# Kernel optimization log

Hardware: AMD Instinct MI355X
Metric: run time of the kernel (lower is better)

Reference implementation:

```python
import jax, jax.numpy as jnp
import numpy as np

VERY_NEG = -1e30


def setup_inputs() -> dict:
    key = jax.random.key(0)
    kq, kk, kv, km = jax.random.split(key, 4)
    B, H, S, D = 4, 8, 2048, 64
    Q = jax.random.normal(kq, (B, H, S, D), dtype=jnp.float32)
    K = jax.random.normal(kk, (B, H, S, D), dtype=jnp.float32)
    V = jax.random.normal(kv, (B, H, S, D), dtype=jnp.float32)
    # key-padding mask broadcast over heads and queries: 1 = keep, 0 = masked
    mask = jax.random.randint(km, (B, 1, 1, S), 0, 2, dtype=jnp.int32)
    return {"Q": Q, "K": K, "V": V, "mask": mask}


def reference(Q, K, V, mask):
    d_k = Q.shape[-1]
    scale = jnp.asarray(np.power(d_k, 0.5), dtype=Q.dtype)
    # scores: [B,H,S_q,S_k]
    scores = jnp.einsum("bhqd,bhkd->bhqk", Q, K) / scale
    # QANet exponential_mask: add -1e30 where mask == 0
    masked = scores + (1.0 - mask.astype(scores.dtype)) * VERY_NEG
    attn = jax.nn.softmax(masked, axis=-1)
    out = jnp.einsum("bhqk,bhkd->bhqd", attn, V)
    return out
```

## Files before the change

### kernel.cpp

```cpp
#include <hip/hip_runtime.h>

typedef _Float16 half8_t __attribute__((ext_vector_type(8)));
typedef _Float16 half4_t __attribute__((ext_vector_type(4)));
typedef _Float16 half2_t __attribute__((ext_vector_type(2)));
typedef __fp16 fp16x2 __attribute__((ext_vector_type(2)));
typedef float f32x4 __attribute__((ext_vector_type(4)));

#define S_LEN 2048
#define D_DIM 64
#define SD (S_LEN * D_DIM)
#define BC 64
#define NKT (S_LEN / BC)
#define LDK 72
#define LDO 68
#define THR 4.0f
#define WS_NEED ((size_t)16 * 1024 * 1024)

__global__ __launch_bounds__(256)
void prep_kernel(const float* __restrict__ Kg, const float* __restrict__ Vg,
                 _Float16* __restrict__ wsK, _Float16* __restrict__ wsV) {
  __shared__ float vt[64][68];
  const int blk = blockIdx.x;
  const int t = threadIdx.x;

  if (blk < 1024) {
    const int bh = blk >> 5, kt = blk & 31;
    const float* src = Kg + (size_t)bh * SD + (size_t)kt * BC * D_DIM;
    char* dst = (char*)wsK + (size_t)blk * 8192;
#pragma unroll
    for (int i = 0; i < 2; ++i) {
      int task = t + 256 * i;
      int row = task >> 3, j = task & 7;
      float4 lo = *(const float4*)(src + row * D_DIM + 8 * j);
      float4 hi = *(const float4*)(src + row * D_DIM + 8 * j + 4);
      fp16x2 p0 = __builtin_amdgcn_cvt_pkrtz(lo.x, lo.y);
      fp16x2 p1 = __builtin_amdgcn_cvt_pkrtz(lo.z, lo.w);
      fp16x2 p2 = __builtin_amdgcn_cvt_pkrtz(hi.x, hi.y);
      fp16x2 p3 = __builtin_amdgcn_cvt_pkrtz(hi.z, hi.w);
      half8_t h;
      h[0] = (_Float16)p0[0]; h[1] = (_Float16)p0[1];
      h[2] = (_Float16)p1[0]; h[3] = (_Float16)p1[1];
      h[4] = (_Float16)p2[0]; h[5] = (_Float16)p2[1];
      h[6] = (_Float16)p3[0]; h[7] = (_Float16)p3[1];
      *(half8_t*)(dst + row * 128 + ((16 * j) ^ ((row & 7) << 4))) = h;
    }
  } else {
    const int vb = blk - 1024;
    const int bh = vb >> 5, kt = vb & 31;
    const float* src = Vg + (size_t)bh * SD + (size_t)kt * BC * D_DIM;
#pragma unroll
    for (int i = 0; i < 4; ++i) {
      int r = (t >> 4) + 16 * i, c4 = t & 15;
      *(float4*)&vt[r][c4 * 4] = *(const float4*)(src + r * D_DIM + c4 * 4);
    }
    __syncthreads();
    char* dst = (char*)wsV + (size_t)vb * 8192;
#pragma unroll
    for (int i = 0; i < 4; ++i) {
      int task = t + 256 * i;
      int drow = task >> 4, j2 = task & 15, k0 = 4 * j2;
      float a = vt[k0][drow], b = vt[k0 + 1][drow];
      float cc = vt[k0 + 2][drow], d = vt[k0 + 3][drow];
      fp16x2 h0 = __builtin_amdgcn_cvt_pkrtz(a, b);
      fp16x2 h1 = __builtin_amdgcn_cvt_pkrtz(cc, d);
      half4_t h;
      h[0] = (_Float16)h0[0]; h[1] = (_Float16)h0[1];
      h[2] = (_Float16)h1[0]; h[3] = (_Float16)h1[1];
      *(half4_t*)(dst + drow * 128 + ((8 * j2) ^ ((drow & 15) << 3))) = h;
    }
  }
}

__global__ __launch_bounds__(256, 2)
void fattn_dma(const float* __restrict__ Qg, const _Float16* __restrict__ wsK,
               const _Float16* __restrict__ wsV, const int* __restrict__ Mg,
               float* __restrict__ Og) {
  __shared__ __align__(16) char smem[40960];
  float* Msh = (float*)(smem + 32768);
  float* Osh = (float*)smem;

  const int t = threadIdx.x;
  const int w = t >> 6;
  const int lane = t & 63;
  const int g = lane >> 4;
  const int c = lane & 15;

  const int bh = blockIdx.x & 31;
  const int qt = blockIdx.x >> 5;
  const int qb = qt * 128;

  const float* Qb = Qg + (size_t)bh * SD;
  const int*   Mb = Mg + (size_t)(bh >> 3) * S_LEN;
  float*       Ob = Og + (size_t)bh * SD;

  {
    int4 m0 = *(const int4*)(Mb + 8 * t);
    int4 m1 = *(const int4*)(Mb + 8 * t + 4);
    float4 f0, f1;
    f0.x = (float)(m0.x - 1) * 1e30f; f0.y = (float)(m0.y - 1) * 1e30f;
    f0.z = (float)(m0.z - 1) * 1e30f; f0.w = (float)(m0.w - 1) * 1e30f;
    f1.x = (float)(m1.x - 1) * 1e30f; f1.y = (float)(m1.y - 1) * 1e30f;
    f1.z = (float)(m1.z - 1) * 1e30f; f1.w = (float)(m1.w - 1) * 1e30f;
    *(float4*)(Msh + 8 * t) = f0;
    *(float4*)(Msh + 8 * t + 4) = f1;
  }

  const float qscale = 0.125f * 1.44269504088896340736f;
  half8_t qf[2][2];
#pragma unroll
  for (int h = 0; h < 2; ++h) {
    const float* qp = Qb + (size_t)(qb + 32 * w + 16 * h + c) * D_DIM + 8 * g;
#pragma unroll
    for (int ks = 0; ks < 2; ++ks) {
      float4 lo = *(const float4*)(qp + 32 * ks);
      float4 hi = *(const float4*)(qp + 32 * ks + 4);
      fp16x2 p0 = __builtin_amdgcn_cvt_pkrtz(lo.x * qscale, lo.y * qscale);
      fp16x2 p1 = __builtin_amdgcn_cvt_pkrtz(lo.z * qscale, lo.w * qscale);
      fp16x2 p2 = __builtin_amdgcn_cvt_pkrtz(hi.x * qscale, hi.y * qscale);
      fp16x2 p3 = __builtin_amdgcn_cvt_pkrtz(hi.z * qscale, hi.w * qscale);
      half8_t hh;
      hh[0] = (_Float16)p0[0]; hh[1] = (_Float16)p0[1];
      hh[2] = (_Float16)p1[0]; hh[3] = (_Float16)p1[1];
      hh[4] = (_Float16)p2[0]; hh[5] = (_Float16)p2[1];
      hh[6] = (_Float16)p3[0]; hh[7] = (_Float16)p3[1];
      qf[h][ks] = hh;
    }
  }

  const size_t tile_base0 = (size_t)bh * 32 * 8192;
  auto dma = [&](int buf, int kt) {
    const char* gK = (const char*)wsK + tile_base0 + (size_t)kt * 8192 +
                     w * 2048 + lane * 16;
    const char* gV = (const char*)wsV + tile_base0 + (size_t)kt * 8192 +
                     w * 2048 + lane * 16;
    char* lK = smem + 8192 * buf + w * 2048;
    char* lV = smem + 16384 + 8192 * buf + w * 2048;
    __builtin_amdgcn_global_load_lds((const float*)gK, (float*)lK, 16, 0, 0);
    __builtin_amdgcn_global_load_lds((const float*)(gK + 1024), (float*)(lK + 1024), 16, 0, 0);
    __builtin_amdgcn_global_load_lds((const float*)gV, (float*)lV, 16, 0, 0);
    __builtin_amdgcn_global_load_lds((const float*)(gV + 1024), (float*)(lV + 1024), 16, 0, 0);
  };

  f32x4 acc[2][4];
  f32x4 accl[2];
#pragma unroll
  for (int h = 0; h < 2; ++h) {
#pragma unroll
    for (int j = 0; j < 4; ++j) accl[h][j] = 0.f;
#pragma unroll
    for (int i = 0; i < 4; ++i)
#pragma unroll
      for (int j = 0; j < 4; ++j) acc[h][i][j] = 0.f;
  }
  float mrun[2] = {-1e30f, -1e30f};

  half4_t ones4;
  ones4[0] = (_Float16)1.0f; ones4[1] = (_Float16)1.0f;
  ones4[2] = (_Float16)1.0f; ones4[3] = (_Float16)1.0f;

  const int kxor = (c & 7) << 4;
  const int vxor = c << 3;

  dma(0, 0);
  __syncthreads();

  for (int kt = 0; kt < NKT; ++kt) {
    const int cur = kt & 1;
    if (kt < NKT - 1) dma(cur ^ 1, kt + 1);

    const char* Kc = smem + 8192 * cur;
    const char* Vc = smem + 16384 + 8192 * cur;

    f32x4 sT[2][4];
    __builtin_amdgcn_s_setprio(1);
#pragma unroll
    for (int mt = 0; mt < 4; ++mt) {
      f32x4 z0, z1;
#pragma unroll
      for (int j = 0; j < 4; ++j) { z0[j] = 0.f; z1[j] = 0.f; }
#pragma unroll
      for (int ks = 0; ks < 2; ++ks) {
        half8_t kf = *(const half8_t*)(Kc + (16 * mt + c) * 128 +
                                       ((ks * 64 + g * 16) ^ kxor));
        z0 = __builtin_amdgcn_mfma_f32_16x16x32_f16(kf, qf[0][ks], z0, 0, 0, 0);
        z1 = __builtin_amdgcn_mfma_f32_16x16x32_f16(kf, qf[1][ks], z1, 0, 0, 0);
      }
      sT[0][mt] = z0;
      sT[1][mt] = z1;
    }
    __builtin_amdgcn_s_setprio(0);

    half4_t vf[4][4];
#pragma unroll
    for (int dt = 0; dt < 4; ++dt)
#pragma unroll
      for (int mtk = 0; mtk < 4; ++mtk)
        vf[dt][mtk] = *(const half4_t*)(Vc + (16 * dt + c) * 128 +
                                        ((mtk * 32 + g * 8) ^ vxor));

    f32x4 mvf[4];
#pragma unroll
    for (int mt = 0; mt < 4; ++mt)
      mvf[mt] = *(const f32x4*)(Msh + kt * BC + 16 * mt + 4 * g);
#pragma unroll
    for (int h = 0; h < 2; ++h)
#pragma unroll
      for (int mt = 0; mt < 4; ++mt)
#pragma unroll
        for (int r = 0; r < 4; ++r) sT[h][mt][r] += mvf[mt][r];

    float tl[2];
#pragma unroll
    for (int h = 0; h < 2; ++h) {
      float tm0 = fmaxf(fmaxf(sT[h][0][0], sT[h][0][1]),
                        fmaxf(sT[h][0][2], sT[h][0][3]));
      float tm1 = fmaxf(fmaxf(sT[h][1][0], sT[h][1][1]),
                        fmaxf(sT[h][1][2], sT[h][1][3]));
      float tm2 = fmaxf(fmaxf(sT[h][2][0], sT[h][2][1]),
                        fmaxf(sT[h][2][2], sT[h][2][3]));
      float tm3 = fmaxf(fmaxf(sT[h][3][0], sT[h][3][1]),
                        fmaxf(sT[h][3][2], sT[h][3][3]));
      tl[h] = fmaxf(fmaxf(tm0, tm1), fmaxf(tm2, tm3));
    }
    int ok0 = __all(tl[0] <= mrun[0] + THR);
    int ok1 = __all(tl[1] <= mrun[1] + THR);
    if (!(ok0 & ok1)) {
#pragma unroll
      for (int h = 0; h < 2; ++h) {
        float tmax = tl[h];
        tmax = fmaxf(tmax, __shfl_xor(tmax, 16));
        tmax = fmaxf(tmax, __shfl_xor(tmax, 32));
        float mnew = fmaxf(mrun[h], tmax);
        float alpha = __builtin_amdgcn_exp2f(mrun[h] - mnew);
        mrun[h] = mnew;
        accl[h][0] *= alpha; accl[h][1] *= alpha;
        accl[h][2] *= alpha; accl[h][3] *= alpha;
#pragma unroll
        for (int mt = 0; mt < 4; ++mt) {
          acc[h][mt][0] *= alpha; acc[h][mt][1] *= alpha;
          acc[h][mt][2] *= alpha; acc[h][mt][3] *= alpha;
        }
      }
    }

    __builtin_amdgcn_s_setprio(1);
#pragma unroll
    for (int h = 0; h < 2; ++h) {
#pragma unroll
      for (int mt = 0; mt < 4; ++mt) {
        float pv0 = __builtin_amdgcn_exp2f(sT[h][mt][0] - mrun[h]);
        float pv1 = __builtin_amdgcn_exp2f(sT[h][mt][1] - mrun[h]);
        float pv2 = __builtin_amdgcn_exp2f(sT[h][mt][2] - mrun[h]);
        float pv3 = __builtin_amdgcn_exp2f(sT[h][mt][3] - mrun[h]);
        fp16x2 p01 = __builtin_amdgcn_cvt_pkrtz(pv0, pv1);
        fp16x2 p23 = __builtin_amdgcn_cvt_pkrtz(pv2, pv3);
        half4_t pf;
        pf[0] = (_Float16)p01[0]; pf[1] = (_Float16)p01[1];
        pf[2] = (_Float16)p23[0]; pf[3] = (_Float16)p23[1];
        accl[h] = __builtin_amdgcn_mfma_f32_16x16x16f16(ones4, pf, accl[h], 0, 0, 0);
#pragma unroll
        for (int dt = 0; dt < 4; ++dt)
          acc[h][dt] = __builtin_amdgcn_mfma_f32_16x16x16f16(vf[dt][mt], pf,
                                                             acc[h][dt], 0, 0, 0);
      }
    }
    __builtin_amdgcn_s_setprio(0);

    __syncthreads();
  }

#pragma unroll
  for (int h = 0; h < 2; ++h) {
    float linv = 1.f / accl[h][0];
#pragma unroll
    for (int mt = 0; mt < 4; ++mt)
#pragma unroll
      for (int r = 0; r < 4; ++r)
        Osh[(32 * w + 16 * h + c) * LDO + 16 * mt + 4 * g + r] = acc[h][mt][r] * linv;
  }
  __syncthreads();
  {
    int f8 = t & 7;
#pragma unroll
    for (int i = 0; i < 4; ++i) {
      int q = (t >> 3) + 32 * i;
#pragma unroll
      for (int j = 0; j < 2; ++j) {
        int c4 = f8 + 8 * j;
        f32x4 o = *(f32x4*)(Osh + q * LDO + c4 * 4);
        *(float4*)(Ob + (size_t)(qb + q) * D_DIM + c4 * 4) =
            make_float4(o.x, o.y, o.z, o.w);
      }
    }
  }
}

__global__ __launch_bounds__(256, 2)
void fattn_fb(const float* __restrict__ Qg, const float* __restrict__ Kg,
              const float* __restrict__ Vg, const int* __restrict__ Mg,
              float* __restrict__ Og) {
  __shared__ __align__(16) char smem[45056];
  float* Msh = (float*)(smem + 36864);
  float* Osh = (float*)smem;

  const int t = threadIdx.x;
  const int w = t >> 6;
  const int lane = t & 63;
  const int g = lane >> 4;
  const int c = lane & 15;

  const int bh = blockIdx.x & 31;
  const int qt = blockIdx.x >> 5;
  const int qb = qt * 128;

  const float* Qb = Qg + (size_t)bh * SD;
  const float* Kb = Kg + (size_t)bh * SD;
  const float* Vb = Vg + (size_t)bh * SD;
  const int*   Mb = Mg + (size_t)(bh >> 3) * S_LEN;
  float*       Ob = Og + (size_t)bh * SD;

  {
    int4 m0 = *(const int4*)(Mb + 8 * t);
    int4 m1 = *(const int4*)(Mb + 8 * t + 4);
    float4 f0, f1;
    f0.x = (float)(m0.x - 1) * 1e30f; f0.y = (float)(m0.y - 1) * 1e30f;
    f0.z = (float)(m0.z - 1) * 1e30f; f0.w = (float)(m0.w - 1) * 1e30f;
    f1.x = (float)(m1.x - 1) * 1e30f; f1.y = (float)(m1.y - 1) * 1e30f;
    f1.z = (float)(m1.z - 1) * 1e30f; f1.w = (float)(m1.w - 1) * 1e30f;
    *(float4*)(Msh + 8 * t) = f0;
    *(float4*)(Msh + 8 * t + 4) = f1;
  }

  const float qscale = 0.125f * 1.44269504088896340736f;
  half8_t qf[2][2];
#pragma unroll
  for (int h = 0; h < 2; ++h) {
    const float* qp = Qb + (size_t)(qb + 32 * w + 16 * h + c) * D_DIM + 8 * g;
#pragma unroll
    for (int ks = 0; ks < 2; ++ks) {
      float4 lo = *(const float4*)(qp + 32 * ks);
      float4 hi = *(const float4*)(qp + 32 * ks + 4);
      fp16x2 p0 = __builtin_amdgcn_cvt_pkrtz(lo.x * qscale, lo.y * qscale);
      fp16x2 p1 = __builtin_amdgcn_cvt_pkrtz(lo.z * qscale, lo.w * qscale);
      fp16x2 p2 = __builtin_amdgcn_cvt_pkrtz(hi.x * qscale, hi.y * qscale);
      fp16x2 p3 = __builtin_amdgcn_cvt_pkrtz(hi.z * qscale, hi.w * qscale);
      half8_t hh;
      hh[0] = (_Float16)p0[0]; hh[1] = (_Float16)p0[1];
      hh[2] = (_Float16)p1[0]; hh[3] = (_Float16)p1[1];
      hh[4] = (_Float16)p2[0]; hh[5] = (_Float16)p2[1];
      hh[6] = (_Float16)p3[0]; hh[7] = (_Float16)p3[1];
      qf[h][ks] = hh;
    }
  }

  const int krow0 = t >> 4;
  const int kc4   = t & 15;
  const int vp    = t >> 3;
  const int vkpl  = t & 7;

  float4 kr[4];
  float2 vr[8];
  auto prefetch = [&](int kb2) {
#pragma unroll
    for (int it = 0; it < 4; ++it)
      kr[it] = *(const float4*)(Kb + (size_t)(kb2 + krow0 + 16 * it) * D_DIM + kc4 * 4);
#pragma unroll
    for (int kc = 0; kc < 4; ++kc) {
      const float* vpp = Vb + (size_t)(kb2 + 2 * (vkpl + 8 * kc)) * D_DIM + 2 * vp;
      vr[2 * kc]     = *(const float2*)(vpp);
      vr[2 * kc + 1] = *(const float2*)(vpp + D_DIM);
    }
  };
  auto stage = [&](int buf) {
    _Float16* Kd = (_Float16*)(smem + 9216 * buf);
    _Float16* Vd = (_Float16*)(smem + 18432 + 9216 * buf);
#pragma unroll
    for (int it = 0; it < 4; ++it) {
      fp16x2 a  = __builtin_amdgcn_cvt_pkrtz(kr[it].x, kr[it].y);
      fp16x2 b2 = __builtin_amdgcn_cvt_pkrtz(kr[it].z, kr[it].w);
      half4_t h;
      h[0] = (_Float16)a[0]; h[1] = (_Float16)a[1];
      h[2] = (_Float16)b2[0]; h[3] = (_Float16)b2[1];
      *(half4_t*)(Kd + (krow0 + 16 * it) * LDK + kc4 * 4) = h;
    }
#pragma unroll
    for (int kc = 0; kc < 4; ++kc) {
      int kp = vkpl + 8 * kc;
      fp16x2 h0 = __builtin_amdgcn_cvt_pkrtz(vr[2 * kc].x, vr[2 * kc + 1].x);
      fp16x2 h1 = __builtin_amdgcn_cvt_pkrtz(vr[2 * kc].y, vr[2 * kc + 1].y);
      half2_t g0; g0[0] = (_Float16)h0[0]; g0[1] = (_Float16)h0[1];
      half2_t g1; g1[0] = (_Float16)h1[0]; g1[1] = (_Float16)h1[1];
      *(half2_t*)(Vd + (2 * vp) * LDK + 2 * kp) = g0;
      *(half2_t*)(Vd + (2 * vp + 1) * LDK + 2 * kp) = g1;
    }
  };

  f32x4 acc[2][4];
  f32x4 accl[2];
#pragma unroll
  for (int h = 0; h < 2; ++h) {
#pragma unroll
    for (int j = 0; j < 4; ++j) accl[h][j] = 0.f;
#pragma unroll
    for (int i = 0; i < 4; ++i)
#pragma unroll
      for (int j = 0; j < 4; ++j) acc[h][i][j] = 0.f;
  }
  float mrun[2] = {-1e30f, -1e30f};

  half4_t ones4;
  ones4[0] = (_Float16)1.0f; ones4[1] = (_Float16)1.0f;
  ones4[2] = (_Float16)1.0f; ones4[3] = (_Float16)1.0f;

  prefetch(0);
  stage(0);
  prefetch(BC);
  __syncthreads();

  for (int kt = 0; kt < NKT; ++kt) {
    const int kb = kt * BC;
    const int cur = kt & 1;

    if (kt < NKT - 1) stage(cur ^ 1);
    if (kt < NKT - 2) prefetch(kb + 2 * BC);

    const _Float16* Kc = (const _Float16*)(smem + 9216 * cur);
    const _Float16* Vc = (const _Float16*)(smem + 18432 + 9216 * cur);

    f32x4 sT[2][4];
    __builtin_amdgcn_s_setprio(1);
#pragma unroll
    for (int mt = 0; mt < 4; ++mt) {
      f32x4 z0, z1;
#pragma unroll
      for (int j = 0; j < 4; ++j) { z0[j] = 0.f; z1[j] = 0.f; }
#pragma unroll
      for (int ks = 0; ks < 2; ++ks) {
        half8_t kf = *(half8_t*)(Kc + (16 * mt + c) * LDK + ks * 32 + 8 * g);
        z0 = __builtin_amdgcn_mfma_f32_16x16x32_f16(kf, qf[0][ks], z0, 0, 0, 0);
        z1 = __builtin_amdgcn_mfma_f32_16x16x32_f16(kf, qf[1][ks], z1, 0, 0, 0);
      }
      sT[0][mt] = z0;
      sT[1][mt] = z1;
    }
    __builtin_amdgcn_s_setprio(0);

    half4_t vf[4][4];
#pragma unroll
    for (int dt = 0; dt < 4; ++dt)
#pragma unroll
      for (int kst = 0; kst < 4; ++kst)
        vf[dt][kst] = *(half4_t*)(Vc + (16 * dt + c) * LDK + 16 * kst + 4 * g);

    f32x4 mvf[4];
#pragma unroll
    for (int mt = 0; mt < 4; ++mt)
      mvf[mt] = *(const f32x4*)(Msh + kb + 16 * mt + 4 * g);
#pragma unroll
    for (int h = 0; h < 2; ++h)
#pragma unroll
      for (int mt = 0; mt < 4; ++mt)
#pragma unroll
        for (int r = 0; r < 4; ++r) sT[h][mt][r] += mvf[mt][r];

    float tl[2];
#pragma unroll
    for (int h = 0; h < 2; ++h) {
      float tm0 = fmaxf(fmaxf(sT[h][0][0], sT[h][0][1]),
                        fmaxf(sT[h][0][2], sT[h][0][3]));
      float tm1 = fmaxf(fmaxf(sT[h][1][0], sT[h][1][1]),
                        fmaxf(sT[h][1][2], sT[h][1][3]));
      float tm2 = fmaxf(fmaxf(sT[h][2][0], sT[h][2][1]),
                        fmaxf(sT[h][2][2], sT[h][2][3]));
      float tm3 = fmaxf(fmaxf(sT[h][3][0], sT[h][3][1]),
                        fmaxf(sT[h][3][2], sT[h][3][3]));
      tl[h] = fmaxf(fmaxf(tm0, tm1), fmaxf(tm2, tm3));
    }
    int ok0 = __all(tl[0] <= mrun[0] + THR);
    int ok1 = __all(tl[1] <= mrun[1] + THR);
    if (!(ok0 & ok1)) {
#pragma unroll
      for (int h = 0; h < 2; ++h) {
        float tmax = tl[h];
        tmax = fmaxf(tmax, __shfl_xor(tmax, 16));
        tmax = fmaxf(tmax, __shfl_xor(tmax, 32));
        float mnew = fmaxf(mrun[h], tmax);
        float alpha = __builtin_amdgcn_exp2f(mrun[h] - mnew);
        mrun[h] = mnew;
        accl[h][0] *= alpha; accl[h][1] *= alpha;
        accl[h][2] *= alpha; accl[h][3] *= alpha;
#pragma unroll
        for (int mt = 0; mt < 4; ++mt) {
          acc[h][mt][0] *= alpha; acc[h][mt][1] *= alpha;
          acc[h][mt][2] *= alpha; acc[h][mt][3] *= alpha;
        }
      }
    }

    __builtin_amdgcn_s_setprio(1);
#pragma unroll
    for (int h = 0; h < 2; ++h) {
#pragma unroll
      for (int mt = 0; mt < 4; ++mt) {
        float pv0 = __builtin_amdgcn_exp2f(sT[h][mt][0] - mrun[h]);
        float pv1 = __builtin_amdgcn_exp2f(sT[h][mt][1] - mrun[h]);
        float pv2 = __builtin_amdgcn_exp2f(sT[h][mt][2] - mrun[h]);
        float pv3 = __builtin_amdgcn_exp2f(sT[h][mt][3] - mrun[h]);
        fp16x2 p01 = __builtin_amdgcn_cvt_pkrtz(pv0, pv1);
        fp16x2 p23 = __builtin_amdgcn_cvt_pkrtz(pv2, pv3);
        half4_t pf;
        pf[0] = (_Float16)p01[0]; pf[1] = (_Float16)p01[1];
        pf[2] = (_Float16)p23[0]; pf[3] = (_Float16)p23[1];
        accl[h] = __builtin_amdgcn_mfma_f32_16x16x16f16(ones4, pf, accl[h], 0, 0, 0);
#pragma unroll
        for (int dt = 0; dt < 4; ++dt)
          acc[h][dt] = __builtin_amdgcn_mfma_f32_16x16x16f16(vf[dt][mt], pf,
                                                             acc[h][dt], 0, 0, 0);
      }
    }
    __builtin_amdgcn_s_setprio(0);

    __syncthreads();
  }

#pragma unroll
  for (int h = 0; h < 2; ++h) {
    float linv = 1.f / accl[h][0];
#pragma unroll
    for (int mt = 0; mt < 4; ++mt)
#pragma unroll
      for (int r = 0; r < 4; ++r)
        Osh[(32 * w + 16 * h + c) * LDO + 16 * mt + 4 * g + r] = acc[h][mt][r] * linv;
  }
  __syncthreads();
  {
    int f8 = t & 7;
#pragma unroll
    for (int i = 0; i < 4; ++i) {
      int q = (t >> 3) + 32 * i;
#pragma unroll
      for (int j = 0; j < 2; ++j) {
        int c4 = f8 + 8 * j;
        f32x4 o = *(f32x4*)(Osh + q * LDO + c4 * 4);
        *(float4*)(Ob + (size_t)(qb + q) * D_DIM + c4 * 4) =
            make_float4(o.x, o.y, o.z, o.w);
      }
    }
  }
}

extern "C" void kernel_launch(void* const* d_in, const int* in_sizes, int n_in,
                              void* d_out, int out_size, void* d_ws, size_t ws_size,
                              hipStream_t stream) {
  (void)in_sizes; (void)n_in; (void)out_size;
  const float* Q = (const float*)d_in[0];
  const float* K = (const float*)d_in[1];
  const float* V = (const float*)d_in[2];
  const int*   M = (const int*)d_in[3];
  float* O = (float*)d_out;

  if (ws_size >= WS_NEED && d_ws != nullptr) {
    _Float16* wsK = (_Float16*)d_ws;
    _Float16* wsV = wsK + (size_t)32 * S_LEN * D_DIM;
    prep_kernel<<<dim3(2048), dim3(256), 0, stream>>>(K, V, wsK, wsV);
    fattn_dma<<<dim3(32 * 16), dim3(256), 0, stream>>>(Q, wsK, wsV, M, O);
  } else {
    fattn_fb<<<dim3(32 * 16), dim3(256), 0, stream>>>(Q, K, V, M, O);
  }
}
```

Baseline: 141.9 us.

## Fold key mask into prepped V and row-sum weights; double key tile to 128

```diff
diff --git a/kernel.cpp b/kernel.cpp
--- a/kernel.cpp
+++ b/kernel.cpp
@@ -9,23 +9,23 @@
 #define S_LEN 2048
 #define D_DIM 64
 #define SD (S_LEN * D_DIM)
-#define BC 64
-#define NKT (S_LEN / BC)
+#define NT16 16
 #define LDK 72
 #define LDO 68
 #define THR 4.0f
-#define WS_NEED ((size_t)16 * 1024 * 1024)
+#define WS_NEED ((size_t)(16 * 1024 * 1024 + 16384))
 
 __global__ __launch_bounds__(256)
 void prep_kernel(const float* __restrict__ Kg, const float* __restrict__ Vg,
-                 _Float16* __restrict__ wsK, _Float16* __restrict__ wsV) {
+                 const int* __restrict__ Mg, _Float16* __restrict__ wsK,
+                 _Float16* __restrict__ wsV, _Float16* __restrict__ wsKeep) {
   __shared__ float vt[64][68];
   const int blk = blockIdx.x;
   const int t = threadIdx.x;
 
   if (blk < 1024) {
     const int bh = blk >> 5, kt = blk & 31;
-    const float* src = Kg + (size_t)bh * SD + (size_t)kt * BC * D_DIM;
+    const float* src = Kg + (size_t)bh * SD + (size_t)kt * 64 * D_DIM;
     char* dst = (char*)wsK + (size_t)blk * 8192;
 #pragma unroll
     for (int i = 0; i < 2; ++i) {
@@ -44,10 +44,11 @@
       h[6] = (_Float16)p3[0]; h[7] = (_Float16)p3[1];
       *(half8_t*)(dst + row * 128 + ((16 * j) ^ ((row & 7) << 4))) = h;
     }
-  } else {
+  } else if (blk < 2048) {
     const int vb = blk - 1024;
     const int bh = vb >> 5, kt = vb & 31;
-    const float* src = Vg + (size_t)bh * SD + (size_t)kt * BC * D_DIM;
+    const float* src = Vg + (size_t)bh * SD + (size_t)kt * 64 * D_DIM;
+    const int* msk = Mg + (size_t)(bh >> 3) * S_LEN + kt * 64;
 #pragma unroll
     for (int i = 0; i < 4; ++i) {
       int r = (t >> 4) + 16 * i, c4 = t & 15;
@@ -59,8 +60,11 @@
     for (int i = 0; i < 4; ++i) {
       int task = t + 256 * i;
       int drow = task >> 4, j2 = task & 15, k0 = 4 * j2;
-      float a = vt[k0][drow], b = vt[k0 + 1][drow];
-      float cc = vt[k0 + 2][drow], d = vt[k0 + 3][drow];
+      int4 mv = *(const int4*)(msk + k0);
+      float a  = vt[k0][drow]     * (float)mv.x;
+      float b  = vt[k0 + 1][drow] * (float)mv.y;
+      float cc = vt[k0 + 2][drow] * (float)mv.z;
+      float d  = vt[k0 + 3][drow] * (float)mv.w;
       fp16x2 h0 = __builtin_amdgcn_cvt_pkrtz(a, b);
       fp16x2 h1 = __builtin_amdgcn_cvt_pkrtz(cc, d);
       half4_t h;
@@ -68,15 +72,25 @@
       h[2] = (_Float16)h1[0]; h[3] = (_Float16)h1[1];
       *(half4_t*)(dst + drow * 128 + ((8 * j2) ^ ((drow & 15) << 3))) = h;
     }
+  } else {
+    const int b = blk - 2048;
+    const int* src = Mg + (size_t)b * S_LEN + 8 * t;
+    int4 m0 = *(const int4*)src;
+    int4 m1 = *(const int4*)(src + 4);
+    half8_t h;
+    h[0] = (_Float16)(float)m0.x; h[1] = (_Float16)(float)m0.y;
+    h[2] = (_Float16)(float)m0.z; h[3] = (_Float16)(float)m0.w;
+    h[4] = (_Float16)(float)m1.x; h[5] = (_Float16)(float)m1.y;
+    h[6] = (_Float16)(float)m1.z; h[7] = (_Float16)(float)m1.w;
+    *(half8_t*)(wsKeep + (size_t)b * S_LEN + 8 * t) = h;
   }
 }
 
 __global__ __launch_bounds__(256, 2)
 void fattn_dma(const float* __restrict__ Qg, const _Float16* __restrict__ wsK,
-               const _Float16* __restrict__ wsV, const int* __restrict__ Mg,
-               float* __restrict__ Og) {
-  __shared__ __align__(16) char smem[40960];
-  float* Msh = (float*)(smem + 32768);
+               const _Float16* __restrict__ wsV,
+               const _Float16* __restrict__ wsKeep, float* __restrict__ Og) {
+  __shared__ __align__(16) char smem[65536];
   float* Osh = (float*)smem;
 
   const int t = threadIdx.x;
@@ -90,20 +104,8 @@
   const int qb = qt * 128;
 
   const float* Qb = Qg + (size_t)bh * SD;
-  const int*   Mb = Mg + (size_t)(bh >> 3) * S_LEN;
   float*       Ob = Og + (size_t)bh * SD;
-
-  {
-    int4 m0 = *(const int4*)(Mb + 8 * t);
-    int4 m1 = *(const int4*)(Mb + 8 * t + 4);
-    float4 f0, f1;
-    f0.x = (float)(m0.x - 1) * 1e30f; f0.y = (float)(m0.y - 1) * 1e30f;
-    f0.z = (float)(m0.z - 1) * 1e30f; f0.w = (float)(m0.w - 1) * 1e30f;
-    f1.x = (float)(m1.x - 1) * 1e30f; f1.y = (float)(m1.y - 1) * 1e30f;
-    f1.z = (float)(m1.z - 1) * 1e30f; f1.w = (float)(m1.w - 1) * 1e30f;
-    *(float4*)(Msh + 8 * t) = f0;
-    *(float4*)(Msh + 8 * t + 4) = f1;
-  }
+  const _Float16* keepB = wsKeep + (size_t)(bh >> 3) * S_LEN;
 
   const float qscale = 0.125f * 1.44269504088896340736f;
   half8_t qf[2][2];
@@ -127,18 +129,22 @@
     }
   }
 
-  const size_t tile_base0 = (size_t)bh * 32 * 8192;
+  const size_t tbase = (size_t)bh * 32 * 8192;
   auto dma = [&](int buf, int kt) {
-    const char* gK = (const char*)wsK + tile_base0 + (size_t)kt * 8192 +
-                     w * 2048 + lane * 16;
-    const char* gV = (const char*)wsV + tile_base0 + (size_t)kt * 8192 +
-                     w * 2048 + lane * 16;
-    char* lK = smem + 8192 * buf + w * 2048;
-    char* lV = smem + 16384 + 8192 * buf + w * 2048;
-    __builtin_amdgcn_global_load_lds((const float*)gK, (float*)lK, 16, 0, 0);
-    __builtin_amdgcn_global_load_lds((const float*)(gK + 1024), (float*)(lK + 1024), 16, 0, 0);
-    __builtin_amdgcn_global_load_lds((const float*)gV, (float*)lV, 16, 0, 0);
-    __builtin_amdgcn_global_load_lds((const float*)(gV + 1024), (float*)(lV + 1024), 16, 0, 0);
+    const char* gK = (const char*)wsK + tbase + (size_t)kt * 16384 +
+                     w * 4096 + lane * 16;
+    const char* gV = (const char*)wsV + tbase + (size_t)kt * 16384 +
+                     w * 4096 + lane * 16;
+    char* lK = smem + 16384 * buf + w * 4096;
+    char* lV = smem + 32768 + 16384 * buf + w * 4096;
+#pragma unroll
+    for (int i = 0; i < 4; ++i)
+      __builtin_amdgcn_global_load_lds((const float*)(gK + 1024 * i),
+                                       (float*)(lK + 1024 * i), 16, 0, 0);
+#pragma unroll
+    for (int i = 0; i < 4; ++i)
+      __builtin_amdgcn_global_load_lds((const float*)(gV + 1024 * i),
+                                       (float*)(lV + 1024 * i), 16, 0, 0);
   };
 
   f32x4 acc[2][4];
@@ -154,34 +160,35 @@
   }
   float mrun[2] = {-1e30f, -1e30f};
 
-  half4_t ones4;
-  ones4[0] = (_Float16)1.0f; ones4[1] = (_Float16)1.0f;
-  ones4[2] = (_Float16)1.0f; ones4[3] = (_Float16)1.0f;
-
   const int kxor = (c & 7) << 4;
   const int vxor = c << 3;
 
   dma(0, 0);
   __syncthreads();
 
-  for (int kt = 0; kt < NKT; ++kt) {
+  for (int kt = 0; kt < NT16; ++kt) {
     const int cur = kt & 1;
-    if (kt < NKT - 1) dma(cur ^ 1, kt + 1);
-
-    const char* Kc = smem + 8192 * cur;
-    const char* Vc = smem + 16384 + 8192 * cur;
-
-    f32x4 sT[2][4];
+    if (kt < NT16 - 1) dma(cur ^ 1, kt + 1);
+
+    const char* Kc = smem + 16384 * cur;
+    const char* Vc = smem + 32768 + 16384 * cur;
+
+    half4_t kA[8];
+#pragma unroll
+    for (int mt = 0; mt < 8; ++mt)
+      kA[mt] = *(const half4_t*)(keepB + kt * 128 + 16 * mt + 4 * g);
+
+    f32x4 sT[2][8];
     __builtin_amdgcn_s_setprio(1);
 #pragma unroll
-    for (int mt = 0; mt < 4; ++mt) {
+    for (int mt = 0; mt < 8; ++mt) {
+      const char* Krow = Kc + ((mt & 4) ? 8192 : 0) + (16 * (mt & 3) + c) * 128;
       f32x4 z0, z1;
 #pragma unroll
       for (int j = 0; j < 4; ++j) { z0[j] = 0.f; z1[j] = 0.f; }
 #pragma unroll
       for (int ks = 0; ks < 2; ++ks) {
-        half8_t kf = *(const half8_t*)(Kc + (16 * mt + c) * 128 +
-                                       ((ks * 64 + g * 16) ^ kxor));
+        half8_t kf = *(const half8_t*)(Krow + ((ks * 64 + g * 16) ^ kxor));
         z0 = __builtin_amdgcn_mfma_f32_16x16x32_f16(kf, qf[0][ks], z0, 0, 0, 0);
         z1 = __builtin_amdgcn_mfma_f32_16x16x32_f16(kf, qf[1][ks], z1, 0, 0, 0);
       }
@@ -190,37 +197,15 @@
     }
     __builtin_amdgcn_s_setprio(0);
 
-    half4_t vf[4][4];
-#pragma unroll
-    for (int dt = 0; dt < 4; ++dt)
-#pragma unroll
-      for (int mtk = 0; mtk < 4; ++mtk)
-        vf[dt][mtk] = *(const half4_t*)(Vc + (16 * dt + c) * 128 +
-                                        ((mtk * 32 + g * 8) ^ vxor));
-
-    f32x4 mvf[4];
-#pragma unroll
-    for (int mt = 0; mt < 4; ++mt)
-      mvf[mt] = *(const f32x4*)(Msh + kt * BC + 16 * mt + 4 * g);
-#pragma unroll
-    for (int h = 0; h < 2; ++h)
-#pragma unroll
-      for (int mt = 0; mt < 4; ++mt)
-#pragma unroll
-        for (int r = 0; r < 4; ++r) sT[h][mt][r] += mvf[mt][r];
-
     float tl[2];
 #pragma unroll
     for (int h = 0; h < 2; ++h) {
-      float tm0 = fmaxf(fmaxf(sT[h][0][0], sT[h][0][1]),
-                        fmaxf(sT[h][0][2], sT[h][0][3]));
-      float tm1 = fmaxf(fmaxf(sT[h][1][0], sT[h][1][1]),
-                        fmaxf(sT[h][1][2], sT[h][1][3]));
-      float tm2 = fmaxf(fmaxf(sT[h][2][0], sT[h][2][1]),
-                        fmaxf(sT[h][2][2], sT[h][2][3]));
-      float tm3 = fmaxf(fmaxf(sT[h][3][0], sT[h][3][1]),
-                        fmaxf(sT[h][3][2], sT[h][3][3]));
-      tl[h] = fmaxf(fmaxf(tm0, tm1), fmaxf(tm2, tm3));
+      float tm = -1e30f;
+#pragma unroll
+      for (int mt = 0; mt < 8; ++mt)
+        tm = fmaxf(tm, fmaxf(fmaxf(sT[h][mt][0], sT[h][mt][1]),
+                             fmaxf(sT[h][mt][2], sT[h][mt][3])));
+      tl[h] = tm;
     }
     int ok0 = __all(tl[0] <= mrun[0] + THR);
     int ok1 = __all(tl[1] <= mrun[1] + THR);
@@ -245,23 +230,35 @@
 
     __builtin_amdgcn_s_setprio(1);
 #pragma unroll
-    for (int h = 0; h < 2; ++h) {
-#pragma unroll
-      for (int mt = 0; mt < 4; ++mt) {
+    for (int mt = 0; mt < 8; ++mt) {
+      const char* Vsub = Vc + ((mt & 4) ? 8192 : 0);
+      half4_t pf[2];
+#pragma unroll
+      for (int h = 0; h < 2; ++h) {
         float pv0 = __builtin_amdgcn_exp2f(sT[h][mt][0] - mrun[h]);
         float pv1 = __builtin_amdgcn_exp2f(sT[h][mt][1] - mrun[h]);
         float pv2 = __builtin_amdgcn_exp2f(sT[h][mt][2] - mrun[h]);
         float pv3 = __builtin_amdgcn_exp2f(sT[h][mt][3] - mrun[h]);
         fp16x2 p01 = __builtin_amdgcn_cvt_pkrtz(pv0, pv1);
         fp16x2 p23 = __builtin_amdgcn_cvt_pkrtz(pv2, pv3);
-        half4_t pf;
-        pf[0] = (_Float16)p01[0]; pf[1] = (_Float16)p01[1];
-        pf[2] = (_Float16)p23[0]; pf[3] = (_Float16)p23[1];
-        accl[h] = __builtin_amdgcn_mfma_f32_16x16x16f16(ones4, pf, accl[h], 0, 0, 0);
-#pragma unroll
-        for (int dt = 0; dt < 4; ++dt)
-          acc[h][dt] = __builtin_amdgcn_mfma_f32_16x16x16f16(vf[dt][mt], pf,
-                                                             acc[h][dt], 0, 0, 0);
+        half4_t ph;
+        ph[0] = (_Float16)p01[0]; ph[1] = (_Float16)p01[1];
+        ph[2] = (_Float16)p23[0]; ph[3] = (_Float16)p23[1];
+        pf[h] = ph;
+      }
+      half4_t vf[4];
+#pragma unroll
+      for (int dt = 0; dt < 4; ++dt)
+        vf[dt] = *(const half4_t*)(Vsub + (16 * dt + c) * 128 +
+                                   ((32 * (mt & 3) + 8 * g) ^ vxor));
+      accl[0] = __builtin_amdgcn_mfma_f32_16x16x16f16(kA[mt], pf[0], accl[0], 0, 0, 0);
+      accl[1] = __builtin_amdgcn_mfma_f32_16x16x16f16(kA[mt], pf[1], accl[1], 0, 0, 0);
+#pragma unroll
+      for (int dt = 0; dt < 4; ++dt) {
+        acc[0][dt] = __builtin_amdgcn_mfma_f32_16x16x16f16(vf[dt], pf[0],
+                                                           acc[0][dt], 0, 0, 0);
+        acc[1][dt] = __builtin_amdgcn_mfma_f32_16x16x16f16(vf[dt], pf[1],
+                                                           acc[1][dt], 0, 0, 0);
       }
     }
     __builtin_amdgcn_s_setprio(0);
@@ -414,15 +411,15 @@
 
   prefetch(0);
   stage(0);
-  prefetch(BC);
+  prefetch(64);
   __syncthreads();
 
-  for (int kt = 0; kt < NKT; ++kt) {
-    const int kb = kt * BC;
+  for (int kt = 0; kt < 32; ++kt) {
+    const int kb = kt * 64;
     const int cur = kt & 1;
 
-    if (kt < NKT - 1) stage(cur ^ 1);
-    if (kt < NKT - 2) prefetch(kb + 2 * BC);
+    if (kt < 31) stage(cur ^ 1);
+    if (kt < 30) prefetch(kb + 128);
 
     const _Float16* Kc = (const _Float16*)(smem + 9216 * cur);
     const _Float16* Vc = (const _Float16*)(smem + 18432 + 9216 * cur);
@@ -562,8 +559,9 @@
   if (ws_size >= WS_NEED && d_ws != nullptr) {
     _Float16* wsK = (_Float16*)d_ws;
     _Float16* wsV = wsK + (size_t)32 * S_LEN * D_DIM;
-    prep_kernel<<<dim3(2048), dim3(256), 0, stream>>>(K, V, wsK, wsV);
-    fattn_dma<<<dim3(32 * 16), dim3(256), 0, stream>>>(Q, wsK, wsV, M, O);
+    _Float16* wsKeep = (_Float16*)((char*)d_ws + 16 * 1024 * 1024);
+    prep_kernel<<<dim3(2052), dim3(256), 0, stream>>>(K, V, M, wsK, wsV, wsKeep);
+    fattn_dma<<<dim3(32 * 16), dim3(256), 0, stream>>>(Q, wsK, wsV, wsKeep, O);
   } else {
     fattn_fb<<<dim3(32 * 16), dim3(256), 0, stream>>>(Q, K, V, M, O);
   }
```

New measurement: 144.3 us. No clear change (+1.8%).
